# Optimization experiments

Hardware: AMD Instinct MI355X
Metric: run time of the kernel (lower is better)

The kernel has to match this reference:

```python
import math
import jax, jax.numpy as jnp
import numpy as np

L = 6          # num_spherical
EDGE_DIM = 64
N_EDGES = 2_000_000


def setup_inputs() -> dict:
    key = jax.random.key(0)
    k1, k2, k3 = jax.random.split(key, 3)
    local_env = jax.random.normal(k1, (N_EDGES, 2, 3), dtype=jnp.float32)
    pair_indices = jax.random.randint(k2, (N_EDGES, 2), 0, 50000, dtype=jnp.int64)
    kernel = jax.random.normal(k3, (L * L, EDGE_DIM), dtype=jnp.float32) * (1.0 / math.sqrt(L * L))
    bias = jnp.zeros((EDGE_DIM,), dtype=jnp.float32)
    return {"local_env": local_env, "pair_indices": pair_indices, "kernel": kernel, "bias": bias}


def _dfact(n):
    # double factorial n!! for odd n (n >= -1)
    return float(math.prod(range(1, n + 1, 2)))


def real_sph_harm(theta, phi, l_max):
    """Real spherical harmonics Y_lm(theta, phi) for l in [0, l_max), m in [-l, l].
    Returns array of shape (E, l_max**2), ordered (l, m=-l..l)."""
    x = jnp.cos(theta)          # (E,)
    s = jnp.sin(theta)          # (E,)
    # associated Legendre P_l^m(x) via standard recurrences (Condon-Shortley phase)
    P = {(0, 0): jnp.ones_like(x)}
    for m in range(1, l_max):
        P[(m, m)] = ((-1.0) ** m) * _dfact(2 * m - 1) * s ** m
    for m in range(0, l_max - 1):
        P[(m + 1, m)] = (2.0 * m + 1.0) * x * P[(m, m)]
    for m in range(0, l_max):
        for l in range(m + 2, l_max):
            P[(l, m)] = ((2.0 * l - 1.0) * x * P[(l - 1, m)] - (l + m - 1.0) * P[(l - 2, m)]) / (l - m)
    cols = []
    for l in range(l_max):
        for m in range(-l, l + 1):
            am = abs(m)
            K = math.sqrt((2 * l + 1) / (4.0 * math.pi) * math.factorial(l - am) / math.factorial(l + am))
            if m == 0:
                cols.append(K * P[(l, 0)])
            elif m > 0:
                cols.append(math.sqrt(2.0) * K * jnp.cos(m * phi) * P[(l, m)])
            else:
                cols.append(math.sqrt(2.0) * K * jnp.sin(am * phi) * P[(l, am)])
    return jnp.stack(cols, axis=-1)  # (E, l_max^2)


def reference(local_env, pair_indices, kernel, bias):
    env = local_env.reshape(-1, 2, 3)
    polar = env[:, 0]   # (E, 3) local polar axis
    edges = env[:, 1]   # (E, 3) edge vector
    # polar angle theta = atan2(|polar x edge|, polar . edge)
    dot_t = jnp.sum(polar * edges, axis=-1)
    cross_t = jnp.linalg.norm(jnp.cross(polar, edges), axis=-1)
    theta = jnp.arctan2(cross_t, dot_t)
    # azimuthal angle phi w.r.t. a fixed vertical reference direction
    # (source code's undefined `vetical`; fixed global z-axis used here)
    edges_proj = edges * jnp.cos(theta)[:, None]
    vertical = jnp.array([0.0, 0.0, 1.0], dtype=local_env.dtype)
    dot_p = jnp.sum(vertical * edges_proj, axis=-1)
    cross_p = jnp.linalg.norm(jnp.cross(polar, edges_proj), axis=-1)
    phi = jnp.arctan2(cross_p, dot_p)
    sph = real_sph_harm(theta, phi, L)          # (E, L^2)
    out = sph @ kernel + bias                   # (E, edge_dim)
    return out, pair_indices
```

## Files before the change

kernel.cpp:

```cpp
#include <hip/hip_runtime.h>
#include <math.h>

#define FOURPI 12.566370614359172

typedef _Float16 f16x8 __attribute__((ext_vector_type(8)));
typedef float    f32x4 __attribute__((ext_vector_type(4)));

__global__ __launch_bounds__(256) void sph_edge_kernel(
    const float* __restrict__ env,
    const int4*  __restrict__ idx4,
    const float* __restrict__ Kmat,
    const float* __restrict__ bias,
    float* __restrict__ out,
    int N, int n4)
{
    __shared__ __align__(16) char U[32768];
    _Float16* Ylds = reinterpret_cast<_Float16*>(U);

    const int tid  = threadIdx.x;
    const int lane = tid & 63;
    const int w    = tid >> 6;
    const int g    = lane >> 4;
    const int c    = lane & 15;
    const int base = blockIdx.x * 256;
    const int valid = (N - base < 256) ? (N - base) : 256;

    float* Cbuf = reinterpret_cast<float*>(U) + w * 1088;

    {
        int i4 = blockIdx.x * 128 + tid;
        if (tid < 128 && i4 < n4) {
            int4 v = idx4[i4];
            float4 f = make_float4((float)v.x, (float)v.y,
                                   (float)v.z, (float)v.w);
            reinterpret_cast<float4*>(out + (size_t)N * 64)[i4] = f;
        }
    }

    f16x8 Bf[4][2];
    #pragma unroll
    for (int nt = 0; nt < 4; ++nt) {
        #pragma unroll
        for (int kt = 0; kt < 2; ++kt) {
            #pragma unroll
            for (int j = 0; j < 8; ++j) {
                int k = kt * 32 + g * 8 + j;
                float v = (k < 36) ? Kmat[k * 64 + nt * 16 + c] : 0.f;
                Bf[nt][kt][j] = (_Float16)v;
            }
        }
    }
    float biasv[4];
    #pragma unroll
    for (int nt = 0; nt < 4; ++nt) biasv[nt] = bias[nt * 16 + c];

    float Y[36];
    if (tid < valid) {
        const float* p6 = env + (size_t)(base + tid) * 6;
        float2 v0 = *reinterpret_cast<const float2*>(p6);
        float2 v1 = *reinterpret_cast<const float2*>(p6 + 2);
        float2 v2 = *reinterpret_cast<const float2*>(p6 + 4);
        float px = v0.x, py = v0.y, pz = v1.x;
        float ex = v1.y, ey = v2.x, ez = v2.y;

        float dot_t = px*ex + py*ey + pz*ez;
        float cxv = py*ez - pz*ey;
        float cyv = pz*ex - px*ez;
        float czv = px*ey - py*ex;
        float cr2 = cxv*cxv + cyv*cyv + czv*czv;
        float cross_t = sqrtf(cr2);
        float r = sqrtf(dot_t*dot_t + cr2);
        float x = 1.f, s = 0.f;
        if (r > 0.f) { x = dot_t / r; s = cross_t / r; }

        float dp = ez * x;
        float cp = fabsf(x) * cross_t;
        float rp = sqrtf(dp*dp + cp*cp);
        float c1 = 1.f, s1 = 0.f;
        if (rp > 0.f) { c1 = dp / rp; s1 = cp / rp; }

        float tc = 2.f * c1;
        float cm1 = c1,            sm1 = s1;
        float cm2 = tc*cm1 - 1.f,  sm2 = tc*sm1;
        float cm3 = tc*cm2 - cm1,  sm3 = tc*sm2 - sm1;
        float cm4 = tc*cm3 - cm2,  sm4 = tc*sm3 - sm2;
        float cm5 = tc*cm4 - cm3,  sm5 = tc*sm4 - sm3;

        float s2 = s*s, s3 = s2*s, s4 = s2*s2, s5 = s4*s;
        float P10 = x;
        float P11 = -s;
        float P20 = 1.5f*x*x - 0.5f;
        float P21 = -3.f*x*s;
        float P22 = 3.f*s2;
        float P30 = (5.f*x*P20 - 2.f*P10) * (1.f/3.f);
        float P31 = (5.f*x*P21 - 3.f*P11) * 0.5f;
        float P32 = 5.f*x*P22;
        float P33 = -15.f*s3;
        float P40 = (7.f*x*P30 - 3.f*P20) * 0.25f;
        float P41 = (7.f*x*P31 - 4.f*P21) * (1.f/3.f);
        float P42 = (7.f*x*P32 - 5.f*P22) * 0.5f;
        float P43 = 7.f*x*P33;
        float P44 = 105.f*s4;
        float P50 = (9.f*x*P40 - 4.f*P30) * 0.2f;
        float P51 = (9.f*x*P41 - 5.f*P31) * 0.25f;
        float P52 = (9.f*x*P42 - 6.f*P32) * (1.f/3.f);
        float P53 = (9.f*x*P43 - 7.f*P33) * 0.5f;
        float P54 = 9.f*x*P44;
        float P55 = -945.f*s5;

        const float SQ2 = 1.4142135623730951f;
        const float K00 = (float)sqrt(1.0/FOURPI);
        const float K10 = (float)sqrt(3.0/FOURPI);
        const float K11 = (float)sqrt(3.0/FOURPI/2.0);
        const float K20 = (float)sqrt(5.0/FOURPI);
        const float K21 = (float)sqrt(5.0/FOURPI/6.0);
        const float K22 = (float)sqrt(5.0/FOURPI/24.0);
        const float K30 = (float)sqrt(7.0/FOURPI);
        const float K31 = (float)sqrt(7.0/FOURPI/12.0);
        const float K32 = (float)sqrt(7.0/FOURPI/120.0);
        const float K33 = (float)sqrt(7.0/FOURPI/720.0);
        const float K40 = (float)sqrt(9.0/FOURPI);
        const float K41 = (float)sqrt(9.0/FOURPI/20.0);
        const float K42 = (float)sqrt(9.0/FOURPI/360.0);
        const float K43 = (float)sqrt(9.0/FOURPI/5040.0);
        const float K44 = (float)sqrt(9.0/FOURPI/40320.0);
        const float K50 = (float)sqrt(11.0/FOURPI);
        const float K51 = (float)sqrt(11.0/FOURPI/30.0);
        const float K52 = (float)sqrt(11.0/FOURPI/840.0);
        const float K53 = (float)sqrt(11.0/FOURPI/20160.0);
        const float K54 = (float)sqrt(11.0/FOURPI/362880.0);
        const float K55 = (float)sqrt(11.0/FOURPI/3628800.0);

        Y[0]  = K00;
        Y[1]  = SQ2*K11*sm1*P11;
        Y[2]  = K10*P10;
        Y[3]  = SQ2*K11*cm1*P11;
        Y[4]  = SQ2*K22*sm2*P22;
        Y[5]  = SQ2*K21*sm1*P21;
        Y[6]  = K20*P20;
        Y[7]  = SQ2*K21*cm1*P21;
        Y[8]  = SQ2*K22*cm2*P22;
        Y[9]  = SQ2*K33*sm3*P33;
        Y[10] = SQ2*K32*sm2*P32;
        Y[11] = SQ2*K31*sm1*P31;
        Y[12] = K30*P30;
        Y[13] = SQ2*K31*cm1*P31;
        Y[14] = SQ2*K32*cm2*P32;
        Y[15] = SQ2*K33*cm3*P33;
        Y[16] = SQ2*K44*sm4*P44;
        Y[17] = SQ2*K43*sm3*P43;
        Y[18] = SQ2*K42*sm2*P42;
        Y[19] = SQ2*K41*sm1*P41;
        Y[20] = K40*P40;
        Y[21] = SQ2*K41*cm1*P41;
        Y[22] = SQ2*K42*cm2*P42;
        Y[23] = SQ2*K43*cm3*P43;
        Y[24] = SQ2*K44*cm4*P44;
        Y[25] = SQ2*K55*sm5*P55;
        Y[26] = SQ2*K54*sm4*P54;
        Y[27] = SQ2*K53*sm3*P53;
        Y[28] = SQ2*K52*sm2*P52;
        Y[29] = SQ2*K51*sm1*P51;
        Y[30] = K50*P50;
        Y[31] = SQ2*K51*cm1*P51;
        Y[32] = SQ2*K52*cm2*P52;
        Y[33] = SQ2*K53*cm3*P53;
        Y[34] = SQ2*K54*cm4*P54;
        Y[35] = SQ2*K55*cm5*P55;
    } else {
        #pragma unroll
        for (int i = 0; i < 36; ++i) Y[i] = 0.f;
    }

    {
        _Float16 yh[64];
        #pragma unroll
        for (int i = 0; i < 36; ++i) yh[i] = (_Float16)Y[i];
        #pragma unroll
        for (int i = 36; i < 64; ++i) yh[i] = (_Float16)0.f;
        #pragma unroll
        for (int s = 0; s < 8; ++s) {
            int slot = s ^ (tid & 7);
            *reinterpret_cast<f16x8*>(&Ylds[tid * 64 + slot * 8]) =
                *reinterpret_cast<const f16x8*>(&yh[s * 8]);
        }
    }
    __syncthreads();

    f16x8 a0[4], a1[4];
    #pragma unroll
    for (int mt = 0; mt < 4; ++mt) {
        const int row = w * 64 + mt * 16 + c;
        const int sw  = row & 7;
        a0[mt] = *reinterpret_cast<const f16x8*>(
            &Ylds[row * 64 + ((0 + g) ^ sw) * 8]);
        a1[mt] = *reinterpret_cast<const f16x8*>(
            &Ylds[row * 64 + ((4 + g) ^ sw) * 8]);
    }
    __syncthreads();

    #pragma unroll
    for (int mt = 0; mt < 4; ++mt) {
        f32x4 acc[4];
        #pragma unroll
        for (int nt = 0; nt < 4; ++nt) {
            f32x4 a = {biasv[nt], biasv[nt], biasv[nt], biasv[nt]};
            a = __builtin_amdgcn_mfma_f32_16x16x32_f16(a0[mt], Bf[nt][0], a, 0, 0, 0);
            a = __builtin_amdgcn_mfma_f32_16x16x32_f16(a1[mt], Bf[nt][1], a, 0, 0, 0);
            acc[nt] = a;
        }

        #pragma unroll
        for (int nt = 0; nt < 4; ++nt) {
            #pragma unroll
            for (int r = 0; r < 4; ++r)
                Cbuf[(g * 4 + r) * 68 + nt * 16 + c] = acc[nt][r];
        }
        __builtin_amdgcn_wave_barrier();

        const int e_chunk = base + w * 64 + mt * 16;
        float4* ob = reinterpret_cast<float4*>(out) + (size_t)e_chunk * 16;
        #pragma unroll
        for (int i = 0; i < 4; ++i) {
            int f4    = i * 64 + lane;
            int e_loc = f4 >> 4;
            int c4    = f4 & 15;
            if (e_chunk + e_loc < N) {
                float4 v = *reinterpret_cast<const float4*>(
                    &Cbuf[e_loc * 68 + c4 * 4]);
                ob[f4] = v;
            }
        }
        __builtin_amdgcn_wave_barrier();
    }
}

extern "C" void kernel_launch(void* const* d_in, const int* in_sizes, int n_in,
                              void* d_out, int out_size, void* d_ws, size_t ws_size,
                              hipStream_t stream) {
    const float* env  = (const float*)d_in[0];
    const int*   idx  = (const int*)d_in[1];
    const float* Kmat = (const float*)d_in[2];
    const float* bias = (const float*)d_in[3];
    float* out = (float*)d_out;

    int N = in_sizes[0] / 6;
    int n4 = in_sizes[1] / 4;

    int blocks = (N + 255) / 256;
    sph_edge_kernel<<<blocks, 256, 0, stream>>>(
        env, (const int4*)idx, Kmat, bias, out, N, n4);
}
```

Baseline: 142.7 us.

## Shrink LDS, use wave-local barriers, and split index conversion into tail blocks

Shrinks the shared Y staging buffer from a 64-half swizzled row to a 40-half padded row, cutting LDS per block from 32 KB to 20 KB. It also sets launch_bounds to 5 blocks per CU to allow higher occupancy. Because each wave only reads rows it wrote itself, the block-wide __syncthreads calls become wave barriers plus explicit LDS waits. The int64-to-float index conversion moves out of every main block into dedicated tail blocks that each handle 1024 int4 elements. Trade-offs: dropping the XOR swizzle may add LDS bank conflicts, and the minimum-occupancy hint may add register pressure.

After: 224.6 us. 1.57x slower.

```diff
diff --git a/kernel.cpp b/kernel.cpp
--- a/kernel.cpp
+++ b/kernel.cpp
@@ -6,18 +6,33 @@
 typedef _Float16 f16x8 __attribute__((ext_vector_type(8)));
 typedef float    f32x4 __attribute__((ext_vector_type(4)));
 
-__global__ __launch_bounds__(256) void sph_edge_kernel(
+__global__ __launch_bounds__(256, 5) void sph_edge_kernel(
     const float* __restrict__ env,
     const int4*  __restrict__ idx4,
     const float* __restrict__ Kmat,
     const float* __restrict__ bias,
     float* __restrict__ out,
-    int N, int n4)
+    int N, int n4, int nb_main)
 {
-    __shared__ __align__(16) char U[32768];
-    _Float16* Ylds = reinterpret_cast<_Float16*>(U);
+    __shared__ __align__(16) _Float16 Ylds[256 * 40];
 
     const int tid  = threadIdx.x;
+
+    if ((int)blockIdx.x >= nb_main) {
+        int tb = blockIdx.x - nb_main;
+        float4* op = reinterpret_cast<float4*>(out + (size_t)N * 64);
+        #pragma unroll
+        for (int j = 0; j < 4; ++j) {
+            int i4 = tb * 1024 + j * 256 + tid;
+            if (i4 < n4) {
+                int4 v = idx4[i4];
+                op[i4] = make_float4((float)v.x, (float)v.y,
+                                     (float)v.z, (float)v.w);
+            }
+        }
+        return;
+    }
+
     const int lane = tid & 63;
     const int w    = tid >> 6;
     const int g    = lane >> 4;
@@ -25,17 +40,7 @@
     const int base = blockIdx.x * 256;
     const int valid = (N - base < 256) ? (N - base) : 256;
 
-    float* Cbuf = reinterpret_cast<float*>(U) + w * 1088;
-
-    {
-        int i4 = blockIdx.x * 128 + tid;
-        if (tid < 128 && i4 < n4) {
-            int4 v = idx4[i4];
-            float4 f = make_float4((float)v.x, (float)v.y,
-                                   (float)v.z, (float)v.w);
-            reinterpret_cast<float4*>(out + (size_t)N * 64)[i4] = f;
-        }
-    }
+    float* Cbuf = reinterpret_cast<float*>(&Ylds[w * 64 * 40]);
 
     f16x8 Bf[4][2];
     #pragma unroll
@@ -173,31 +178,33 @@
     }
 
     {
-        _Float16 yh[64];
+        _Float16 yh[40];
         #pragma unroll
         for (int i = 0; i < 36; ++i) yh[i] = (_Float16)Y[i];
         #pragma unroll
-        for (int i = 36; i < 64; ++i) yh[i] = (_Float16)0.f;
-        #pragma unroll
-        for (int s = 0; s < 8; ++s) {
-            int slot = s ^ (tid & 7);
-            *reinterpret_cast<f16x8*>(&Ylds[tid * 64 + slot * 8]) =
-                *reinterpret_cast<const f16x8*>(&yh[s * 8]);
-        }
-    }
-    __syncthreads();
+        for (int i = 36; i < 40; ++i) yh[i] = (_Float16)0.f;
+        f16x8* yr = reinterpret_cast<f16x8*>(&Ylds[tid * 40]);
+        #pragma unroll
+        for (int s5 = 0; s5 < 5; ++s5)
+            yr[s5] = *reinterpret_cast<const f16x8*>(&yh[s5 * 8]);
+    }
+    __builtin_amdgcn_wave_barrier();
+    asm volatile("s_waitcnt lgkmcnt(0)" ::: "memory");
+    __builtin_amdgcn_sched_barrier(0);
 
     f16x8 a0[4], a1[4];
     #pragma unroll
     for (int mt = 0; mt < 4; ++mt) {
         const int row = w * 64 + mt * 16 + c;
-        const int sw  = row & 7;
-        a0[mt] = *reinterpret_cast<const f16x8*>(
-            &Ylds[row * 64 + ((0 + g) ^ sw) * 8]);
-        a1[mt] = *reinterpret_cast<const f16x8*>(
-            &Ylds[row * 64 + ((4 + g) ^ sw) * 8]);
-    }
-    __syncthreads();
+        a0[mt] = *reinterpret_cast<const f16x8*>(&Ylds[row * 40 + g * 8]);
+        f16x8 t = {};
+        if (g == 0)
+            t = *reinterpret_cast<const f16x8*>(&Ylds[row * 40 + 32]);
+        a1[mt] = t;
+    }
+    __builtin_amdgcn_wave_barrier();
+    asm volatile("s_waitcnt lgkmcnt(0)" ::: "memory");
+    __builtin_amdgcn_sched_barrier(0);
 
     #pragma unroll
     for (int mt = 0; mt < 4; ++mt) {
@@ -244,10 +251,11 @@
     const float* bias = (const float*)d_in[3];
     float* out = (float*)d_out;
 
-    int N = in_sizes[0] / 6;
+    int N  = in_sizes[0] / 6;
     int n4 = in_sizes[1] / 4;
 
-    int blocks = (N + 255) / 256;
-    sph_edge_kernel<<<blocks, 256, 0, stream>>>(
-        env, (const int4*)idx, Kmat, bias, out, N, n4);
+    int nb_main = (N + 255) / 256;
+    int nb_idx  = (n4 + 1023) / 1024;
+    sph_edge_kernel<<<nb_main + nb_idx, 256, 0, stream>>>(
+        env, (const int4*)idx, Kmat, bias, out, N, n4, nb_main);
 }
```
